# Kernel tuning notes

Measured on AMD Instinct MI355X. Metric: run time of the kernel, lower is better.

Reference implementation:

```python
import jax, jax.numpy as jnp
import numpy as np

DIM = 256
RATIO = 4
SCALE = 8
B, H, W = 16, 128, 128
EPS = 1e-5


def _conv(x, w, pad):
    return jax.lax.conv_general_dilated(
        x, w, window_strides=(1, 1), padding=[(pad, pad), (pad, pad)],
        dimension_numbers=('NCHW', 'OIHW', 'NCHW'))


def _haar_dwt(x):
    # pywt.dwt2(x, 'haar') on even-sized inputs == strided 2x2 sum/difference
    a = x[:, :, 0::2, 0::2]
    b = x[:, :, 0::2, 1::2]
    c = x[:, :, 1::2, 0::2]
    d = x[:, :, 1::2, 1::2]
    ll = (a + b + c + d) * 0.5
    lh = (a + b - c - d) * 0.5  # cH: high-pass along rows
    hl = (a - b + c - d) * 0.5  # cV: high-pass along cols
    hh = (a - b - c + d) * 0.5  # cD
    return jnp.concatenate([ll, lh, hl, hh], axis=1)


def setup_inputs() -> dict:
    key = jax.random.key(0)
    ks = jax.random.split(key, 16)
    dq = DIM // RATIO
    ds = DIM // SCALE
    s = 0.05
    return {
        'x': jax.random.normal(ks[0], (B, DIM, H, W), jnp.float32),
        'reduce_w': jax.random.normal(ks[1], (dq, DIM, 1, 1), jnp.float32) * s,
        'reduce_b': jnp.zeros((dq,), jnp.float32),
        'bn_g': jnp.ones((dq,), jnp.float32),
        'bn_b': jnp.zeros((dq,), jnp.float32),
        'bn_mean': jnp.zeros((dq,), jnp.float32),
        'bn_var': jnp.ones((dq,), jnp.float32),
        'conv_w': jax.random.normal(ks[2], (1, DIM, 1, 1), jnp.float32) * s,
        'conv1_w': jax.random.normal(ks[3], (DIM, DIM, 1, 1), jnp.float32) * s,
        'conv2_w': jax.random.normal(ks[4], (DIM, DIM, 3, 3), jnp.float32) * s,
        'conv3_w': jax.random.normal(ks[5], (DIM, DIM, 5, 5), jnp.float32) * s,
        'conv4_w': jax.random.normal(ks[6], (DIM, DIM, 7, 7), jnp.float32) * s,
        'channel_conv_w': jax.random.normal(ks[7], (DIM, DIM, 3, 3), jnp.float32) * s,
        'conv1x1_w': jax.random.normal(ks[8], (DIM, 6 * DIM, 3, 3), jnp.float32) * s,
        'ct1_w': jax.random.normal(ks[9], (ds, DIM, 1, 1), jnp.float32) * s,
        'ct1_b': jnp.zeros((ds,), jnp.float32),
        'ln_g': jnp.ones((ds,), jnp.float32),
        'ln_b': jnp.zeros((ds,), jnp.float32),
        'ct2_w': jax.random.normal(ks[10], (DIM, ds, 1, 1), jnp.float32) * s,
        'ct2_b': jnp.zeros((DIM,), jnp.float32),
        'proj_w': jax.random.normal(ks[11], (DIM, DIM, 1, 1), jnp.float32) * s,
    }


def reference(x, reduce_w, reduce_b, bn_g, bn_b, bn_mean, bn_var, conv_w,
              conv1_w, conv2_w, conv3_w, conv4_w, channel_conv_w, conv1x1_w,
              ct1_w, ct1_b, ln_g, ln_b, ct2_w, ct2_b, proj_w):
    # max-pool 2x2 stride 2
    p = jax.lax.reduce_window(x, -jnp.inf, jax.lax.max,
                              (1, 1, 2, 2), (1, 1, 2, 2), 'VALID')
    # reduce: 1x1 conv -> BN (inference) -> ReLU
    r = _conv(x, reduce_w, 0) + reduce_b[None, :, None, None]
    r = (r - bn_mean[None, :, None, None]) * jax.lax.rsqrt(bn_var + EPS)[None, :, None, None]
    r = jax.nn.relu(r * bn_g[None, :, None, None] + bn_b[None, :, None, None])
    # Haar DWT (original runs under no_grad: detached from autograd)
    qkv0 = jax.lax.stop_gradient(_haar_dwt(r))  # [B, DIM, H/2, W/2]
    qkv1 = _conv(qkv0, conv1_w, 0)
    qkv2 = _conv(qkv0, conv2_w, 1)
    qkv3 = _conv(qkv0, conv3_w, 2)
    qkv4 = _conv(qkv0, conv4_w, 3)
    qkv = _conv(jnp.concatenate([qkv0, qkv1, qkv2, qkv3, qkv4, p], axis=1),
                conv1x1_w, 1)  # [B, DIM, H/2, W/2]
    n = (H // 2) * (W // 2)
    # spatial attention weights: softmax over spatial positions
    content = _conv(qkv, conv_w, 0).reshape(B, n)          # [B, N]
    content = jax.nn.softmax(content, axis=1)
    channel = _conv(qkv, channel_conv_w, 1).reshape(B, DIM, n)  # [B, C, N]
    pooled = jnp.einsum('bcn,bn->bc', channel, content)[:, :, None, None]
    # channel transform: 1x1 -> LayerNorm over (C,1,1) -> ReLU -> 1x1
    t = _conv(pooled, ct1_w, 0) + ct1_b[None, :, None, None]
    mu = jnp.mean(t, axis=(1, 2, 3), keepdims=True)
    var = jnp.mean(jnp.square(t - mu), axis=(1, 2, 3), keepdims=True)
    t = (t - mu) * jax.lax.rsqrt(var + EPS)
    t = jax.nn.relu(t * ln_g[None, :, None, None] + ln_b[None, :, None, None])
    cw = _conv(t, ct2_w, 0) + ct2_b[None, :, None, None]  # [B, DIM, 1, 1]
    return _conv(qkv * cw, proj_w, 0)
```

## Files before the change

kernel.cpp:

```cpp
#include <hip/hip_runtime.h>
#include <stdint.h>


typedef __attribute__((ext_vector_type(8))) short bf16x8;
typedef __attribute__((ext_vector_type(4))) float f32x4;

#define EPS_ 1e-5f

#define GLOAD16(gp, lp)                                                        \
  __builtin_amdgcn_global_load_lds(                                            \
      (const __attribute__((address_space(1))) void*)(gp),                     \
      (__attribute__((address_space(3))) void*)(lp), 16, 0, 0)

__device__ __forceinline__ float bf2f(unsigned short u) {
  union { unsigned int u; float f; } c; c.u = ((unsigned int)u) << 16; return c.f;
}
__device__ __forceinline__ unsigned short f2bf(float f) {
  union { float f; unsigned int u; } c; c.f = f;
  return (unsigned short)((c.u + 0x7fffu + ((c.u >> 16) & 1u)) >> 16);
}
__device__ __forceinline__ void unpack8(uint4 v, float* f) {
  f[0]=bf2f((unsigned short)(v.x&0xffffu)); f[1]=bf2f((unsigned short)(v.x>>16));
  f[2]=bf2f((unsigned short)(v.y&0xffffu)); f[3]=bf2f((unsigned short)(v.y>>16));
  f[4]=bf2f((unsigned short)(v.z&0xffffu)); f[5]=bf2f((unsigned short)(v.z>>16));
  f[6]=bf2f((unsigned short)(v.w&0xffffu)); f[7]=bf2f((unsigned short)(v.w>>16));
}
__device__ __forceinline__ uint4 pack8(const float* f) {
  uint4 v;
  v.x = (unsigned)f2bf(f[0]) | ((unsigned)f2bf(f[1])<<16);
  v.y = (unsigned)f2bf(f[2]) | ((unsigned)f2bf(f[3])<<16);
  v.z = (unsigned)f2bf(f[4]) | ((unsigned)f2bf(f[5])<<16);
  v.w = (unsigned)f2bf(f[6]) | ((unsigned)f2bf(f[7])<<16);
  return v;
}

__global__ void k_repack(const float* __restrict__ src, unsigned short* __restrict__ dst,
                         int O, int Opad, int I, int T) {
  int gid = blockIdx.x * 256 + threadIdx.x;
  if (gid >= Opad * I * T) return;
  int i = gid % I; int r = gid / I; int o = r % Opad; int t = r / Opad;
  dst[gid] = (o < O) ? f2bf(src[((size_t)(o * I + i)) * T + t]) : (unsigned short)0;
}

__global__ void k_border_zero(unsigned short* __restrict__ buf, int PW, int PB, int C) {
  int IW = PW - 2 * PB;
  int nb = PW * PW - IW * IW;
  int per = C >> 3;
  int gid = blockIdx.x * 256 + threadIdx.x;
  if (gid >= 16 * nb * per) return;
  int cq = gid % per; int r = gid / per; int p = r % nb; int b = r / nb;
  int y, x;
  int top = PB * PW;
  if (p < top) { y = p / PW; x = p - y * PW; }
  else if (p < top + IW * 2 * PB) {
    int q = p - top; y = PB + q / (2 * PB); int rr = q % (2 * PB);
    x = (rr < PB) ? rr : (IW + rr);
  } else { int q = p - top - IW * 2 * PB; y = PB + IW + q / PW; x = q - (q / PW) * PW; }
  uint4 z; z.x = z.y = z.z = z.w = 0u;
  *(uint4*)&buf[(((size_t)b * PW + y) * PW + x) * C + cq * 8] = z;
}

__global__ void k_transpose_x(const float* __restrict__ x, unsigned short* __restrict__ xh) {
  int by = blockIdx.x; int b = by >> 7; int y = by & 127;
  int tid = threadIdx.x;
  __shared__ unsigned short lds[32 * 129];
  for (int c0 = 0; c0 < 256; c0 += 32) {
    #pragma unroll
    for (int i = 0; i < 16; ++i) {
      int e = i * 256 + tid; int ci = e >> 7, xx = e & 127;
      float v = x[(((size_t)b * 256 + c0 + ci) * 128 + y) * 128 + xx];
      lds[ci * 129 + xx] = f2bf(v);
    }
    __syncthreads();
    #pragma unroll
    for (int i2 = 0; i2 < 2; ++i2) {
      int e = i2 * 256 + tid; int pix = e >> 2, q = e & 3;
      unsigned int w0, w1, w2, w3;
      w0 = (unsigned)lds[(q*8+0)*129 + pix] | ((unsigned)lds[(q*8+1)*129 + pix] << 16);
      w1 = (unsigned)lds[(q*8+2)*129 + pix] | ((unsigned)lds[(q*8+3)*129 + pix] << 16);
      w2 = (unsigned)lds[(q*8+4)*129 + pix] | ((unsigned)lds[(q*8+5)*129 + pix] << 16);
      w3 = (unsigned)lds[(q*8+6)*129 + pix] | ((unsigned)lds[(q*8+7)*129 + pix] << 16);
      uint4 v; v.x = w0; v.y = w1; v.z = w2; v.w = w3;
      *(uint4*)&xh[(((size_t)b * 128 + y) * 128 + pix) * 256 + c0 + q * 8] = v;
    }
    __syncthreads();
  }
}

__global__ void k_maxpool(const unsigned short* __restrict__ xh, unsigned short* __restrict__ cat) {
  int gid = blockIdx.x * 256 + threadIdx.x;
  int cq = gid & 31; int pix = gid >> 5;
  int bb = pix >> 12; int yx = pix & 4095;
  int y = yx >> 6, xx2 = yx & 63;
  size_t base = (((size_t)bb * 128 + 2 * y) * 128 + 2 * xx2) * 256 + cq * 8;
  uint4 v00 = *(const uint4*)(xh + base);
  uint4 v01 = *(const uint4*)(xh + base + 256);
  uint4 v10 = *(const uint4*)(xh + base + 32768);
  uint4 v11 = *(const uint4*)(xh + base + 32768 + 256);
  float a[8], b8[8], c8[8], d8[8], m8[8];
  unpack8(v00, a); unpack8(v01, b8); unpack8(v10, c8); unpack8(v11, d8);
  #pragma unroll
  for (int j = 0; j < 8; ++j) m8[j] = fmaxf(fmaxf(a[j], b8[j]), fmaxf(c8[j], d8[j]));
  *(uint4*)(cat + (((size_t)bb * 4900 + (y + 3) * 70 + (xx2 + 3))) * 1536 + 1280 + cq * 8) = pack8(m8);
}

__global__ void k_haar(const unsigned short* __restrict__ rbn, unsigned short* __restrict__ cat) {
  int gid = blockIdx.x * 256 + threadIdx.x;
  int cq = gid & 7; int pix = gid >> 3;
  int bb = pix >> 12; int yx = pix & 4095;
  int y = yx >> 6, xx = yx & 63;
  size_t base = (((size_t)bb * 128 + 2 * y) * 128 + 2 * xx) * 64 + cq * 8;
  uint4 va = *(const uint4*)(rbn + base);
  uint4 vb = *(const uint4*)(rbn + base + 64);
  uint4 vc = *(const uint4*)(rbn + base + 8192);
  uint4 vd = *(const uint4*)(rbn + base + 8192 + 64);
  float a[8], b8[8], c8[8], d8[8], o[8];
  unpack8(va, a); unpack8(vb, b8); unpack8(vc, c8); unpack8(vd, d8);
  size_t ob = ((size_t)bb * 4900 + (y + 3) * 70 + (xx + 3)) * 1536 + cq * 8;
  #pragma unroll
  for (int j = 0; j < 8; ++j) o[j] = (a[j] + b8[j] + c8[j] + d8[j]) * 0.5f;
  *(uint4*)(cat + ob + 0)   = pack8(o);
  #pragma unroll
  for (int j = 0; j < 8; ++j) o[j] = (a[j] + b8[j] - c8[j] - d8[j]) * 0.5f;
  *(uint4*)(cat + ob + 64)  = pack8(o);
  #pragma unroll
  for (int j = 0; j < 8; ++j) o[j] = (a[j] - b8[j] + c8[j] - d8[j]) * 0.5f;
  *(uint4*)(cat + ob + 128) = pack8(o);
  #pragma unroll
  for (int j = 0; j < 8; ++j) o[j] = (a[j] - b8[j] - c8[j] + d8[j]) * 0.5f;
  *(uint4*)(cat + ob + 192) = pack8(o);
}

__global__ __launch_bounds__(512, 1) void k_conv_gemm256(
    const unsigned short* __restrict__ Wt, const unsigned short* __restrict__ Bf,
    int Cin, int Cstr, int cbase,
    int PW, int PB, int KH, int pad,
    unsigned long long wbstride,
    unsigned short* __restrict__ outb, int OCstr, int ocbase, int OPW, int OPB,
    float* __restrict__ outf, int mode) {
  const int tid = threadIdx.x, lane = tid & 63, w = tid >> 6;
  const int wm = w >> 2, wn = w & 3;
  const int nidx = (blockIdx.x & 7) * 32 + (blockIdx.x >> 3);
  const int bn = (nidx & 15) * 256;
  const int b = nidx >> 4;
  if (wbstride) Wt += (size_t)b * wbstride;
  extern __shared__ unsigned short S[];

  f32x4 zero4 = {0.f, 0.f, 0.f, 0.f};
  f32x4 acc[8][4];
  #pragma unroll
  for (int i = 0; i < 8; ++i)
    #pragma unroll
    for (int j = 0; j < 4; ++j) acc[i][j] = zero4;

  const int lq = lane >> 3, lc = lane & 7;
  const int lg = (lc - lq) & 7;
  const int pr = lg >> 2;
  const int ks = lg & 3;
  const unsigned short* aSt = Wt + (size_t)(w * 32 + 2 * lq + pr) * Cin + ks * 8;
  const size_t jA = (size_t)16 * Cin;
  const size_t bimg = (size_t)b * PW * PW;
  const unsigned short* bSt0; const unsigned short* bSt1;
  {
    int p = bn + w * 32 + 2 * lq + pr;
    bSt0 = Bf + (bimg + (size_t)((p >> 6) + PB) * PW + ((p & 63) + PB)) * Cstr + cbase + ks * 8;
    p += 16;
    bSt1 = Bf + (bimg + (size_t)((p >> 6) + PB) * PW + ((p & 63) + PB)) * Cstr + cbase + ks * 8;
  }
  const int dstA0 = w * 1024;
  const int dstB0 = 8192 + w * 1024;

  const int r = lane & 15, s4 = lane >> 4;
  const int ck = (((r & 1) * 4 + s4) + ((r >> 1) & 7)) & 7;
  const int lb = (r >> 1) * 64 + ck * 8;
  const int aOff = wm * 4096 + lb;
  const int bOff = 8192 + wn * 2048 + lb;

  const size_t MC = (size_t)256 * Cin;
  const int NT = (KH * KH * Cin) >> 5;

  const long long t0B = ((long long)(-pad) * PW + (-pad)) * (long long)Cstr;
  GLOAD16(aSt,             S + dstA0);
  GLOAD16(aSt + jA,        S + dstA0 + 512);
  GLOAD16(bSt0 + t0B,      S + dstB0);
  GLOAD16(bSt1 + t0B,      S + dstB0 + 512);
  GLOAD16(aSt + 32,        S + 16384 + dstA0);
  GLOAD16(aSt + jA + 32,   S + 16384 + dstA0 + 512);
  GLOAD16(bSt0 + t0B + 32, S + 16384 + dstB0);
  GLOAD16(bSt1 + t0B + 32, S + 16384 + dstB0 + 512);
  asm volatile("s_waitcnt vmcnt(4)" ::: "memory");
  __builtin_amdgcn_s_barrier();
  __builtin_amdgcn_sched_barrier(0);

  int kc2 = 64, ty2 = 0, tx2 = 0;
  for (int t = 0; t < NT; ++t) {
    const unsigned short* Sc = S + (t & 3) * 16384;
    unsigned short* Sn = (unsigned short*)S + ((t + 2) & 3) * 16384;
    const bool hn = (t + 2) < NT;
    long long offA = 0, offB = 0;
    if (hn) {
      offA = (long long)(ty2 * KH + tx2) * MC + kc2;
      offB = ((long long)(ty2 - pad) * PW + (tx2 - pad)) * (long long)Cstr + kc2;
      kc2 += 32;
      if (kc2 == Cin) { kc2 = 0; ++tx2; if (tx2 == KH) { tx2 = 0; ++ty2; } }
    }
    bf16x8 a[4], bb[4];
    #pragma unroll
    for (int mi = 0; mi < 4; ++mi) a[mi] = *(const bf16x8*)(Sc + aOff + mi * 512);
    #pragma unroll
    for (int ni = 0; ni < 4; ++ni) bb[ni] = *(const bf16x8*)(Sc + bOff + ni * 512);
    if (hn) {
      GLOAD16(aSt + offA,      Sn + dstA0);
      GLOAD16(aSt + jA + offA, Sn + dstA0 + 512);
    }
    __builtin_amdgcn_s_setprio(1);
    #pragma unroll
    for (int mi = 0; mi < 4; ++mi)
      #pragma unroll
      for (int ni = 0; ni < 4; ++ni)
        acc[mi][ni] = __builtin_amdgcn_mfma_f32_16x16x32_bf16(a[mi], bb[ni], acc[mi][ni], 0, 0, 0);
    __builtin_amdgcn_s_setprio(0);
    __builtin_amdgcn_s_barrier();
    #pragma unroll
    for (int mi = 0; mi < 4; ++mi) a[mi] = *(const bf16x8*)(Sc + aOff + (mi + 4) * 512);
    if (hn) {
      GLOAD16(bSt0 + offB, Sn + dstB0);
      GLOAD16(bSt1 + offB, Sn + dstB0 + 512);
    }
    __builtin_amdgcn_s_setprio(1);
    #pragma unroll
    for (int mi = 0; mi < 4; ++mi)
      #pragma unroll
      for (int ni = 0; ni < 4; ++ni)
        acc[mi + 4][ni] = __builtin_amdgcn_mfma_f32_16x16x32_bf16(a[mi], bb[ni], acc[mi + 4][ni], 0, 0, 0);
    __builtin_amdgcn_s_setprio(0);
    if (t + 1 < NT) {
      if (t + 2 < NT) { asm volatile("s_waitcnt vmcnt(4)" ::: "memory"); }
      else            { asm volatile("s_waitcnt vmcnt(0)" ::: "memory"); }
      __builtin_amdgcn_s_barrier();
      __builtin_amdgcn_sched_barrier(0);
    }
  }

  const size_t bimgO = (size_t)b * OPW * OPW;
  #pragma unroll
  for (int mi = 0; mi < 8; ++mi) {
    const int mf = wm * 128 + mi * 16 + (lane >> 4) * 4;
    #pragma unroll
    for (int ni = 0; ni < 4; ++ni) {
      const int n = bn + wn * 64 + ni * 16 + (lane & 15);
      if (mode == 2) {
        #pragma unroll
        for (int vv = 0; vv < 4; ++vv)
          outf[((size_t)b * 256 + mf + vv) * 4096 + n] = acc[mi][ni][vv];
      } else {
        const int oy = n >> 6, ox = n & 63;
        unsigned short h[4];
        #pragma unroll
        for (int vv = 0; vv < 4; ++vv) h[vv] = f2bf(acc[mi][ni][vv]);
        uint2 st; st.x = (unsigned)h[0] | ((unsigned)h[1] << 16);
        st.y = (unsigned)h[2] | ((unsigned)h[3] << 16);
        *(uint2*)&outb[(bimgO + (size_t)(oy + OPB) * OPW + (ox + OPB)) * OCstr + ocbase + mf] = st;
      }
    }
  }
}

__global__ __launch_bounds__(256) void k_conv_gemm(
    const unsigned short* __restrict__ Wt, const unsigned short* __restrict__ Bf,
    int M, int Mpad, int Cin, int Cstr, int cbase,
    int OW, int lgOW, int PW, int PB, int KH, int pad,
    unsigned long long wbstride,
    unsigned short* __restrict__ outb, int OCstr, int ocbase, int OPW, int OPB,
    float* __restrict__ outf, int mode,
    const float* __restrict__ rb, const float* __restrict__ bng, const float* __restrict__ bnb,
    const float* __restrict__ bnm, const float* __restrict__ bnv) {
  const int tid = threadIdx.x, lane = tid & 63, w = tid >> 6;
  const int wm = w >> 1, wn = w & 1;
  const int bm = blockIdx.y * 128, bn = blockIdx.x * 128;
  const int b = blockIdx.z;
  const int Npix = OW * OW;
  if (wbstride) Wt += (size_t)b * wbstride;

  __shared__ __align__(1024) unsigned short sA[128 * 32];
  __shared__ __align__(1024) unsigned short sB[128 * 32];

  f32x4 zero4 = {0.f, 0.f, 0.f, 0.f};
  f32x4 acc[4][4];
  #pragma unroll
  for (int i = 0; i < 4; ++i)
    #pragma unroll
    for (int j = 0; j < 4; ++j) acc[i][j] = zero4;

  const int srow = lane >> 2;
  const int slog = (lane & 3) ^ ((lane >> 3) & 3);
// ... 80 lines not shown
        *(uint2*)&outb[(bimgO + (size_t)(oy + OPB) * OPW + (ox + OPB)) * OCstr + ocbase + mf] = st;
      }
    }
  }
}

__global__ void k_content_logits(const unsigned short* __restrict__ qkv,
                                 const float* __restrict__ conv_w,
                                 float* __restrict__ logits) {
  int j = blockIdx.x, b = blockIdx.y, tid = threadIdx.x;
  __shared__ float wl[256];
  wl[tid] = conv_w[tid];
  __syncthreads();
  int pl = tid >> 3, kp = tid & 7;
  #pragma unroll
  for (int pass = 0; pass < 4; ++pass) {
    int p = j * 128 + pass * 32 + pl;
    int y = p >> 6, x = p & 63;
    const unsigned short* q = qkv + (((size_t)b * 66 + y + 1) * 66 + (x + 1)) * 256 + kp * 32;
    float s = 0.f;
    #pragma unroll
    for (int i = 0; i < 32; i += 8) {
      uint4 v = *(const uint4*)(q + i);
      float f[8]; unpack8(v, f);
      #pragma unroll
      for (int k = 0; k < 8; ++k) s += f[k] * wl[kp * 32 + i + k];
    }
    s += __shfl_down(s, 4, 8);
    s += __shfl_down(s, 2, 8);
    s += __shfl_down(s, 1, 8);
    if (kp == 0) logits[(size_t)b * 4096 + p] = s;
  }
}

__global__ void k_softmax4096(float* __restrict__ cont) {
  int b = blockIdx.x, tid = threadIdx.x;
  __shared__ float red[256];
  float sv[16]; float mx = -1e30f;
  #pragma unroll
  for (int j = 0; j < 16; ++j) { sv[j] = cont[(size_t)b * 4096 + j * 256 + tid]; mx = fmaxf(mx, sv[j]); }
  red[tid] = mx; __syncthreads();
  for (int s = 128; s > 0; s >>= 1) { if (tid < s) red[tid] = fmaxf(red[tid], red[tid + s]); __syncthreads(); }
  mx = red[0]; __syncthreads();
  float sum = 0.f;
  #pragma unroll
  for (int j = 0; j < 16; ++j) { sv[j] = expf(sv[j] - mx); sum += sv[j]; }
  red[tid] = sum; __syncthreads();
  for (int s = 128; s > 0; s >>= 1) { if (tid < s) red[tid] += red[tid + s]; __syncthreads(); }
  float inv = 1.f / red[0];
  #pragma unroll
  for (int j = 0; j < 16; ++j) cont[(size_t)b * 4096 + j * 256 + tid] = sv[j] * inv;
}

__global__ void k_pooled_part(const unsigned short* __restrict__ chn,
                              const float* __restrict__ content, float* __restrict__ ppart) {
  int j = blockIdx.x, b = blockIdx.y, c = threadIdx.x;
  const unsigned short* base = chn + (size_t)b * 4096 * 256 + c;
  const float* ct = content + (size_t)b * 4096;
  float acc = 0.f;
  int n0 = j * 128;
  for (int n = n0; n < n0 + 128; ++n)
    acc += bf2f(base[(size_t)n * 256]) * ct[n];
  ppart[((size_t)b * 32 + j) * 256 + c] = acc;
}
__global__ void k_pooled_red(const float* __restrict__ ppart, float* __restrict__ pooled) {
  int b = blockIdx.x, c = threadIdx.x;
  float s = 0.f;
  #pragma unroll
  for (int j = 0; j < 32; ++j) s += ppart[((size_t)b * 32 + j) * 256 + c];
  pooled[b * 256 + c] = s;
}

__global__ void k_ct(const float* __restrict__ pooled,
                     const float* __restrict__ ct1w, const float* __restrict__ ct1b,
                     const float* __restrict__ lng, const float* __restrict__ lnb,
                     const float* __restrict__ ct2w, const float* __restrict__ ct2b,
                     float* __restrict__ cw) {
  int b = blockIdx.x, tid = threadIdx.x;
  __shared__ float tt[32];
  __shared__ float stats[2];
  if (tid < 32) {
    float s = 0.f;
    const float* w = ct1w + tid * 256;
    const float* p = pooled + b * 256;
    for (int i = 0; i < 256; ++i) s += w[i] * p[i];
    tt[tid] = s + ct1b[tid];
  }
  __syncthreads();
  if (tid == 0) {
    float mu = 0.f;
    for (int j = 0; j < 32; ++j) mu += tt[j];
    mu *= (1.f / 32.f);
    float va = 0.f;
    for (int j = 0; j < 32; ++j) { float d = tt[j] - mu; va += d * d; }
    va *= (1.f / 32.f);
    stats[0] = mu; stats[1] = rsqrtf(va + EPS_);
  }
  __syncthreads();
  if (tid < 32) {
    float v = (tt[tid] - stats[0]) * stats[1];
    tt[tid] = fmaxf(v * lng[tid] + lnb[tid], 0.f);
  }
  __syncthreads();
  float s = 0.f;
  const float* w2 = ct2w + tid * 32;
  #pragma unroll
  for (int j = 0; j < 32; ++j) s += w2[j] * tt[j];
  cw[b * 256 + tid] = s + ct2b[tid];
}

__global__ void k_aproj(const float* __restrict__ projw, const float* __restrict__ cw,
                        unsigned short* __restrict__ aproj) {
  int gid = blockIdx.x * 256 + threadIdx.x;
  int b = gid >> 16; int oi = gid & 65535; int i = oi & 255;
  aproj[gid] = f2bf(projw[oi] * cw[b * 256 + i]);
}

extern "C" void kernel_launch(void* const* d_in, const int* in_sizes, int n_in,
                              void* d_out, int out_size, void* d_ws, size_t ws_size,
                              hipStream_t stream) {
  (void)in_sizes; (void)n_in; (void)out_size; (void)ws_size;
  const float* x        = (const float*)d_in[0];
  const float* reduce_w = (const float*)d_in[1];
  const float* reduce_b = (const float*)d_in[2];
  const float* bn_g     = (const float*)d_in[3];
  const float* bn_b     = (const float*)d_in[4];
  const float* bn_mean  = (const float*)d_in[5];
  const float* bn_var   = (const float*)d_in[6];
  const float* conv_w   = (const float*)d_in[7];
  const float* conv1_w  = (const float*)d_in[8];
  const float* conv2_w  = (const float*)d_in[9];
  const float* conv3_w  = (const float*)d_in[10];
  const float* conv4_w  = (const float*)d_in[11];
  const float* chconv_w = (const float*)d_in[12];
  const float* cat_w    = (const float*)d_in[13];
  const float* ct1_w    = (const float*)d_in[14];
  const float* ct1_b    = (const float*)d_in[15];
  const float* ln_g     = (const float*)d_in[16];
  const float* ln_b     = (const float*)d_in[17];
  const float* ct2_w    = (const float*)d_in[18];
  const float* ct2_b    = (const float*)d_in[19];
  const float* proj_w   = (const float*)d_in[20];

  static bool attr_done = false;
  if (!attr_done) {
    hipFuncSetAttribute(reinterpret_cast<const void*>(&k_conv_gemm256),
                        hipFuncAttributeMaxDynamicSharedMemorySize, 131072);
    attr_done = true;
  }

  char* wsp = (char*)d_ws;
  size_t off = 0;
  auto alloc = [&](size_t bytes) -> char* {
    char* p = wsp + off; off += (bytes + 255) & ~(size_t)255; return p;
  };
  unsigned short* XH    = (unsigned short*)alloc((size_t)16 * 16384 * 256 * 2);
  unsigned short* CAT   = (unsigned short*)alloc((size_t)16 * 4900 * 1536 * 2);
  unsigned short* RBN   = (unsigned short*)alloc((size_t)16 * 16384 * 64 * 2);
  unsigned short* CHN   = RBN;
  unsigned short* QKV   = (unsigned short*)alloc((size_t)16 * 4356 * 256 * 2);
  float*          CONT  = (float*)alloc((size_t)16 * 4096 * 4);
  float*          PPART = (float*)alloc((size_t)16 * 32 * 256 * 4);
  float*          POOL  = (float*)alloc(16 * 256 * 4);
  float*          CWB   = (float*)alloc(16 * 256 * 4);
  unsigned short* WR    = (unsigned short*)alloc((size_t)128 * 256 * 2);
  unsigned short* W1    = (unsigned short*)alloc((size_t)256 * 256 * 2);
  unsigned short* W2    = (unsigned short*)alloc((size_t)9 * 256 * 256 * 2);
  unsigned short* W3    = (unsigned short*)alloc((size_t)25 * 256 * 256 * 2);
  unsigned short* W4    = (unsigned short*)alloc((size_t)49 * 256 * 256 * 2);
  unsigned short* WC    = (unsigned short*)alloc((size_t)9 * 256 * 256 * 2);
  unsigned short* WCAT  = (unsigned short*)alloc((size_t)9 * 256 * 1536 * 2);
  unsigned short* APROJ = (unsigned short*)alloc((size_t)16 * 256 * 256 * 2);

  auto rp = [&](const float* s, unsigned short* d, int O, int Opad, int I, int T) {
    int tot = Opad * I * T;
    k_repack<<<(tot + 255) / 256, 256, 0, stream>>>(s, d, O, Opad, I, T);
  };
  rp(reduce_w, WR, 64, 128, 256, 1);
  rp(conv1_w, W1, 256, 256, 256, 1);
  rp(conv2_w, W2, 256, 256, 256, 9);
  rp(conv3_w, W3, 256, 256, 256, 25);
  rp(conv4_w, W4, 256, 256, 256, 49);
  rp(chconv_w, WC, 256, 256, 256, 9);
  rp(cat_w, WCAT, 256, 256, 1536, 9);

  k_border_zero<<<(16 * 804 * 192 + 255) / 256, 256, 0, stream>>>(CAT, 70, 3, 1536);
  k_border_zero<<<(16 * 260 * 32 + 255) / 256, 256, 0, stream>>>(QKV, 66, 1, 256);

  k_transpose_x<<<2048, 256, 0, stream>>>(x, XH);
  k_maxpool<<<8192, 256, 0, stream>>>(XH, CAT);

  dim3 blk(256);
  k_conv_gemm<<<dim3(128, 1, 16), blk, 0, stream>>>(WR, XH, 64, 128, 256, 256, 0,
      128, 7, 128, 0, 1, 0, 0ULL, RBN, 64, 0, 128, 0, nullptr, 1,
      reduce_b, bn_g, bn_b, bn_mean, bn_var);
  k_haar<<<2048, 256, 0, stream>>>(RBN, CAT);
  k_conv_gemm256<<<256, 512, 131072, stream>>>(W1, CAT, 256, 1536, 0,
      70, 3, 1, 0, 0ULL, CAT, 1536, 256, 70, 3, nullptr, 0);
  k_conv_gemm256<<<256, 512, 131072, stream>>>(W2, CAT, 256, 1536, 0,
      70, 3, 3, 1, 0ULL, CAT, 1536, 512, 70, 3, nullptr, 0);
  k_conv_gemm256<<<256, 512, 131072, stream>>>(W3, CAT, 256, 1536, 0,
      70, 3, 5, 2, 0ULL, CAT, 1536, 768, 70, 3, nullptr, 0);
  k_conv_gemm256<<<256, 512, 131072, stream>>>(W4, CAT, 256, 1536, 0,
      70, 3, 7, 3, 0ULL, CAT, 1536, 1024, 70, 3, nullptr, 0);
  k_conv_gemm256<<<256, 512, 131072, stream>>>(WCAT, CAT, 1536, 1536, 0,
      70, 3, 3, 1, 0ULL, QKV, 256, 0, 66, 1, nullptr, 0);
  k_content_logits<<<dim3(32, 16), blk, 0, stream>>>(QKV, conv_w, CONT);
  k_softmax4096<<<16, blk, 0, stream>>>(CONT);
  k_conv_gemm256<<<256, 512, 131072, stream>>>(WC, QKV, 256, 256, 0,
      66, 1, 3, 1, 0ULL, CHN, 256, 0, 64, 0, nullptr, 0);
  k_pooled_part<<<dim3(32, 16), blk, 0, stream>>>(CHN, CONT, PPART);
  k_pooled_red<<<16, blk, 0, stream>>>(PPART, POOL);
  k_ct<<<16, blk, 0, stream>>>(POOL, ct1_w, ct1_b, ln_g, ln_b, ct2_w, ct2_b, CWB);
  k_aproj<<<4096, 256, 0, stream>>>(proj_w, CWB, APROJ);
  k_conv_gemm256<<<256, 512, 131072, stream>>>(APROJ, QKV, 256, 256, 0,
      66, 1, 1, 0, 65536ULL, nullptr, 256, 0, 64, 0, (float*)d_out, 2);
}
```

Measured before the change: 1.459 ms.

## Shrink conv GEMM tiles to 256x128 with 256 threads and two blocks per CU

Changes the main implicit-GEMM conv kernel from 512-thread blocks computing 256x256 tiles with a 4-stage dynamic LDS ring to 256-thread blocks computing 256x128 tiles with a static double-buffered LDS of 48KB. The aim is two resident blocks per CU and twice as many blocks per launch, which should improve latency hiding and load balance. The prefetch now waits on vmcnt(0) every iteration and keeps only one stage in flight, so memory latency may be less well hidden. The B tile is reused across half as many output channels per load, raising global traffic relative to compute.

```diff
diff --git a/kernel.cpp b/kernel.cpp
--- a/kernel.cpp
+++ b/kernel.cpp
@@ -131,7 +131,7 @@
   *(uint4*)(cat + ob + 192) = pack8(o);
 }
 
-__global__ __launch_bounds__(512, 1) void k_conv_gemm256(
+__global__ __launch_bounds__(256, 2) void k_conv_gemm256(
     const unsigned short* __restrict__ Wt, const unsigned short* __restrict__ Bf,
     int Cin, int Cstr, int cbase,
     int PW, int PB, int KH, int pad,
@@ -139,12 +139,12 @@
     unsigned short* __restrict__ outb, int OCstr, int ocbase, int OPW, int OPB,
     float* __restrict__ outf, int mode) {
   const int tid = threadIdx.x, lane = tid & 63, w = tid >> 6;
-  const int wm = w >> 2, wn = w & 3;
-  const int nidx = (blockIdx.x & 7) * 32 + (blockIdx.x >> 3);
-  const int bn = (nidx & 15) * 256;
-  const int b = nidx >> 4;
+  const int wm = w >> 1, wn = w & 1;
+  const int swz = (blockIdx.x & 7) * 64 + (blockIdx.x >> 3);
+  const int bn = (swz & 31) * 128;
+  const int b = swz >> 5;
   if (wbstride) Wt += (size_t)b * wbstride;
-  extern __shared__ unsigned short S[];
+  __shared__ __align__(1024) unsigned short S[24576];
 
   f32x4 zero4 = {0.f, 0.f, 0.f, 0.f};
   f32x4 acc[8][4];
@@ -157,7 +157,7 @@
   const int lg = (lc - lq) & 7;
   const int pr = lg >> 2;
   const int ks = lg & 3;
-  const unsigned short* aSt = Wt + (size_t)(w * 32 + 2 * lq + pr) * Cin + ks * 8;
+  const unsigned short* aSt = Wt + (size_t)(w * 64 + 2 * lq + pr) * Cin + ks * 8;
   const size_t jA = (size_t)16 * Cin;
   const size_t bimg = (size_t)b * PW * PW;
   const unsigned short* bSt0; const unsigned short* bSt1;
@@ -167,8 +167,8 @@
     p += 16;
     bSt1 = Bf + (bimg + (size_t)((p >> 6) + PB) * PW + ((p & 63) + PB)) * Cstr + cbase + ks * 8;
   }
-  const int dstA0 = w * 1024;
-  const int dstB0 = 8192 + w * 1024;
+  const int dA = w * 2048;
+  const int dB = 8192 + w * 1024;
 
   const int r = lane & 15, s4 = lane >> 4;
   const int ck = (((r & 1) * 4 + s4) + ((r >> 1) & 7)) & 7;
@@ -180,63 +180,47 @@
   const int NT = (KH * KH * Cin) >> 5;
 
   const long long t0B = ((long long)(-pad) * PW + (-pad)) * (long long)Cstr;
-  GLOAD16(aSt,             S + dstA0);
-  GLOAD16(aSt + jA,        S + dstA0 + 512);
-  GLOAD16(bSt0 + t0B,      S + dstB0);
-  GLOAD16(bSt1 + t0B,      S + dstB0 + 512);
-  GLOAD16(aSt + 32,        S + 16384 + dstA0);
-  GLOAD16(aSt + jA + 32,   S + 16384 + dstA0 + 512);
-  GLOAD16(bSt0 + t0B + 32, S + 16384 + dstB0);
-  GLOAD16(bSt1 + t0B + 32, S + 16384 + dstB0 + 512);
-  asm volatile("s_waitcnt vmcnt(4)" ::: "memory");
+  GLOAD16(aSt,            S + dA);
+  GLOAD16(aSt + jA,       S + dA + 512);
+  GLOAD16(aSt + 2 * jA,   S + dA + 1024);
+  GLOAD16(aSt + 3 * jA,   S + dA + 1536);
+  GLOAD16(bSt0 + t0B,     S + dB);
+  GLOAD16(bSt1 + t0B,     S + dB + 512);
+  asm volatile("s_waitcnt vmcnt(0)" ::: "memory");
   __builtin_amdgcn_s_barrier();
   __builtin_amdgcn_sched_barrier(0);
 
-  int kc2 = 64, ty2 = 0, tx2 = 0;
+  int kcn = 0, tyn = 0, txn = 0;
   for (int t = 0; t < NT; ++t) {
-    const unsigned short* Sc = S + (t & 3) * 16384;
-    unsigned short* Sn = (unsigned short*)S + ((t + 2) & 3) * 16384;
-    const bool hn = (t + 2) < NT;
-    long long offA = 0, offB = 0;
+    const unsigned short* Sc = S + (t & 1) * 12288;
+    unsigned short* Sn = (unsigned short*)S + ((t + 1) & 1) * 12288;
+    const bool hn = (t + 1) < NT;
     if (hn) {
-      offA = (long long)(ty2 * KH + tx2) * MC + kc2;
-      offB = ((long long)(ty2 - pad) * PW + (tx2 - pad)) * (long long)Cstr + kc2;
-      kc2 += 32;
-      if (kc2 == Cin) { kc2 = 0; ++tx2; if (tx2 == KH) { tx2 = 0; ++ty2; } }
-    }
-    bf16x8 a[4], bb[4];
-    #pragma unroll
-    for (int mi = 0; mi < 4; ++mi) a[mi] = *(const bf16x8*)(Sc + aOff + mi * 512);
+      kcn += 32;
+      if (kcn == Cin) { kcn = 0; ++txn; if (txn == KH) { txn = 0; ++tyn; } }
+      const long long offA = (long long)(tyn * KH + txn) * MC + kcn;
+      const long long offB = ((long long)(tyn - pad) * PW + (txn - pad)) * (long long)Cstr + kcn;
+      GLOAD16(aSt + offA,          Sn + dA);
+      GLOAD16(aSt + offA + jA,     Sn + dA + 512);
+      GLOAD16(aSt + offA + 2 * jA, Sn + dA + 1024);
+      GLOAD16(aSt + offA + 3 * jA, Sn + dA + 1536);
+      GLOAD16(bSt0 + offB,         Sn + dB);
+      GLOAD16(bSt1 + offB,         Sn + dB + 512);
+    }
+    bf16x8 a[8], bb[4];
+    #pragma unroll
+    for (int mi = 0; mi < 8; ++mi) a[mi] = *(const bf16x8*)(Sc + aOff + mi * 512);
     #pragma unroll
     for (int ni = 0; ni < 4; ++ni) bb[ni] = *(const bf16x8*)(Sc + bOff + ni * 512);
-    if (hn) {
-      GLOAD16(aSt + offA,      Sn + dstA0);
-      GLOAD16(aSt + jA + offA, Sn + dstA0 + 512);
-    }
     __builtin_amdgcn_s_setprio(1);
     #pragma unroll
-    for (int mi = 0; mi < 4; ++mi)
+    for (int mi = 0; mi < 8; ++mi)
       #pragma unroll
       for (int ni = 0; ni < 4; ++ni)
         acc[mi][ni] = __builtin_amdgcn_mfma_f32_16x16x32_bf16(a[mi], bb[ni], acc[mi][ni], 0, 0, 0);
     __builtin_amdgcn_s_setprio(0);
-    __builtin_amdgcn_s_barrier();
-    #pragma unroll
-    for (int mi = 0; mi < 4; ++mi) a[mi] = *(const bf16x8*)(Sc + aOff + (mi + 4) * 512);
     if (hn) {
-      GLOAD16(bSt0 + offB, Sn + dstB0);
-      GLOAD16(bSt1 + offB, Sn + dstB0 + 512);
-    }
-    __builtin_amdgcn_s_setprio(1);
-    #pragma unroll
-    for (int mi = 0; mi < 4; ++mi)
-      #pragma unroll
-      for (int ni = 0; ni < 4; ++ni)
-        acc[mi + 4][ni] = __builtin_amdgcn_mfma_f32_16x16x32_bf16(a[mi], bb[ni], acc[mi + 4][ni], 0, 0, 0);
-    __builtin_amdgcn_s_setprio(0);
-    if (t + 1 < NT) {
-      if (t + 2 < NT) { asm volatile("s_waitcnt vmcnt(4)" ::: "memory"); }
-      else            { asm volatile("s_waitcnt vmcnt(0)" ::: "memory"); }
+      asm volatile("s_waitcnt vmcnt(0)" ::: "memory");
       __builtin_amdgcn_s_barrier();
       __builtin_amdgcn_sched_barrier(0);
     }
@@ -517,13 +501,6 @@
   const float* ct2_b    = (const float*)d_in[19];
   const float* proj_w   = (const float*)d_in[20];
 
-  static bool attr_done = false;
-  if (!attr_done) {
-    hipFuncSetAttribute(reinterpret_cast<const void*>(&k_conv_gemm256),
-                        hipFuncAttributeMaxDynamicSharedMemorySize, 131072);
-    attr_done = true;
-  }
-
   char* wsp = (char*)d_ws;
   size_t off = 0;
   auto alloc = [&](size_t bytes) -> char* {
@@ -570,24 +547,24 @@
       128, 7, 128, 0, 1, 0, 0ULL, RBN, 64, 0, 128, 0, nullptr, 1,
       reduce_b, bn_g, bn_b, bn_mean, bn_var);
   k_haar<<<2048, 256, 0, stream>>>(RBN, CAT);
-  k_conv_gemm256<<<256, 512, 131072, stream>>>(W1, CAT, 256, 1536, 0,
+  k_conv_gemm256<<<512, 256, 0, stream>>>(W1, CAT, 256, 1536, 0,
       70, 3, 1, 0, 0ULL, CAT, 1536, 256, 70, 3, nullptr, 0);
-  k_conv_gemm256<<<256, 512, 131072, stream>>>(W2, CAT, 256, 1536, 0,
+  k_conv_gemm256<<<512, 256, 0, stream>>>(W2, CAT, 256, 1536, 0,
       70, 3, 3, 1, 0ULL, CAT, 1536, 512, 70, 3, nullptr, 0);
-  k_conv_gemm256<<<256, 512, 131072, stream>>>(W3, CAT, 256, 1536, 0,
+  k_conv_gemm256<<<512, 256, 0, stream>>>(W3, CAT, 256, 1536, 0,
       70, 3, 5, 2, 0ULL, CAT, 1536, 768, 70, 3, nullptr, 0);
-  k_conv_gemm256<<<256, 512, 131072, stream>>>(W4, CAT, 256, 1536, 0,
+  k_conv_gemm256<<<512, 256, 0, stream>>>(W4, CAT, 256, 1536, 0,
       70, 3, 7, 3, 0ULL, CAT, 1536, 1024, 70, 3, nullptr, 0);
-  k_conv_gemm256<<<256, 512, 131072, stream>>>(WCAT, CAT, 1536, 1536, 0,
+  k_conv_gemm256<<<512, 256, 0, stream>>>(WCAT, CAT, 1536, 1536, 0,
       70, 3, 3, 1, 0ULL, QKV, 256, 0, 66, 1, nullptr, 0);
   k_content_logits<<<dim3(32, 16), blk, 0, stream>>>(QKV, conv_w, CONT);
   k_softmax4096<<<16, blk, 0, stream>>>(CONT);
-  k_conv_gemm256<<<256, 512, 131072, stream>>>(WC, QKV, 256, 256, 0,
+  k_conv_gemm256<<<512, 256, 0, stream>>>(WC, QKV, 256, 256, 0,
       66, 1, 3, 1, 0ULL, CHN, 256, 0, 64, 0, nullptr, 0);
   k_pooled_part<<<dim3(32, 16), blk, 0, stream>>>(CHN, CONT, PPART);
   k_pooled_red<<<16, blk, 0, stream>>>(PPART, POOL);
   k_ct<<<16, blk, 0, stream>>>(POOL, ct1_w, ct1_b, ln_g, ln_b, ct2_w, ct2_b, CWB);
   k_aproj<<<4096, 256, 0, stream>>>(proj_w, CWB, APROJ);
-  k_conv_gemm256<<<256, 512, 131072, stream>>>(APROJ, QKV, 256, 256, 0,
+  k_conv_gemm256<<<512, 256, 0, stream>>>(APROJ, QKV, 256, 256, 0,
       66, 1, 1, 0, 65536ULL, nullptr, 256, 0, 64, 0, (float*)d_out, 2);
 }
```

Measured after the change: 1.564 ms. 1.07x slower.

## Deepen GEMM pipeline to three LDS stages with register-double-buffered fragments

Applied to the files above, without the earlier changes.

Restructures the conv-GEMM main loop to prefetch three K-tiles ahead into the four-slot LDS ring. It also double-buffers the A/B MFMA fragments in registers, so the next tile's LDS reads overlap the current tile's MFMAs. The per-tile barrier count drops from two to one. Launch bounds are raised to request two blocks per CU. With 128 accumulator floats plus two full fragment sets, this risks heavy register spilling, and the 128KB LDS footprint likely prevents the second block from fitting anyway.

```diff
diff --git a/kernel.cpp b/kernel.cpp
--- a/kernel.cpp
+++ b/kernel.cpp
@@ -131,7 +131,7 @@
   *(uint4*)(cat + ob + 192) = pack8(o);
 }
 
-__global__ __launch_bounds__(512, 1) void k_conv_gemm256(
+__global__ __launch_bounds__(512, 2) void k_conv_gemm256(
     const unsigned short* __restrict__ Wt, const unsigned short* __restrict__ Bf,
     int Cin, int Cstr, int cbase,
     int PW, int PB, int KH, int pad,
@@ -144,7 +144,7 @@
   const int bn = (nidx & 15) * 256;
   const int b = nidx >> 4;
   if (wbstride) Wt += (size_t)b * wbstride;
-  extern __shared__ unsigned short S[];
+  extern __shared__ unsigned short Sb[];
 
   f32x4 zero4 = {0.f, 0.f, 0.f, 0.f};
   f32x4 acc[8][4];
@@ -167,8 +167,8 @@
     p += 16;
     bSt1 = Bf + (bimg + (size_t)((p >> 6) + PB) * PW + ((p & 63) + PB)) * Cstr + cbase + ks * 8;
   }
-  const int dstA0 = w * 1024;
-  const int dstB0 = 8192 + w * 1024;
+  const int dA = w * 1024;
+  const int dB = 8192 + w * 1024;
 
   const int r = lane & 15, s4 = lane >> 4;
   const int ck = (((r & 1) * 4 + s4) + ((r >> 1) & 7)) & 7;
@@ -180,67 +180,73 @@
   const int NT = (KH * KH * Cin) >> 5;
 
   const long long t0B = ((long long)(-pad) * PW + (-pad)) * (long long)Cstr;
-  GLOAD16(aSt,             S + dstA0);
-  GLOAD16(aSt + jA,        S + dstA0 + 512);
-  GLOAD16(bSt0 + t0B,      S + dstB0);
-  GLOAD16(bSt1 + t0B,      S + dstB0 + 512);
-  GLOAD16(aSt + 32,        S + 16384 + dstA0);
-  GLOAD16(aSt + jA + 32,   S + 16384 + dstA0 + 512);
-  GLOAD16(bSt0 + t0B + 32, S + 16384 + dstB0);
-  GLOAD16(bSt1 + t0B + 32, S + 16384 + dstB0 + 512);
+  #pragma unroll
+  for (int j = 0; j < 3; ++j) {
+    unsigned short* Sw = Sb + j * 16384;
+    GLOAD16(aSt + j * 32,        Sw + dA);
+    GLOAD16(aSt + j * 32 + jA,   Sw + dA + 512);
+    GLOAD16(bSt0 + t0B + j * 32, Sw + dB);
+    GLOAD16(bSt1 + t0B + j * 32, Sw + dB + 512);
+  }
   asm volatile("s_waitcnt vmcnt(4)" ::: "memory");
   __builtin_amdgcn_s_barrier();
   __builtin_amdgcn_sched_barrier(0);
 
-  int kc2 = 64, ty2 = 0, tx2 = 0;
-  for (int t = 0; t < NT; ++t) {
-    const unsigned short* Sc = S + (t & 3) * 16384;
-    unsigned short* Sn = (unsigned short*)S + ((t + 2) & 3) * 16384;
-    const bool hn = (t + 2) < NT;
-    long long offA = 0, offB = 0;
-    if (hn) {
-      offA = (long long)(ty2 * KH + tx2) * MC + kc2;
-      offB = ((long long)(ty2 - pad) * PW + (tx2 - pad)) * (long long)Cstr + kc2;
-      kc2 += 32;
-      if (kc2 == Cin) { kc2 = 0; ++tx2; if (tx2 == KH) { tx2 = 0; ++ty2; } }
-    }
-    bf16x8 a[4], bb[4];
-    #pragma unroll
-    for (int mi = 0; mi < 4; ++mi) a[mi] = *(const bf16x8*)(Sc + aOff + mi * 512);
-    #pragma unroll
-    for (int ni = 0; ni < 4; ++ni) bb[ni] = *(const bf16x8*)(Sc + bOff + ni * 512);
-    if (hn) {
-      GLOAD16(aSt + offA,      Sn + dstA0);
-      GLOAD16(aSt + jA + offA, Sn + dstA0 + 512);
-    }
-    __builtin_amdgcn_s_setprio(1);
-    #pragma unroll
-    for (int mi = 0; mi < 4; ++mi)
-      #pragma unroll
-      for (int ni = 0; ni < 4; ++ni)
-        acc[mi][ni] = __builtin_amdgcn_mfma_f32_16x16x32_bf16(a[mi], bb[ni], acc[mi][ni], 0, 0, 0);
-    __builtin_amdgcn_s_setprio(0);
-    __builtin_amdgcn_s_barrier();
-    #pragma unroll
-    for (int mi = 0; mi < 4; ++mi) a[mi] = *(const bf16x8*)(Sc + aOff + (mi + 4) * 512);
-    if (hn) {
-      GLOAD16(bSt0 + offB, Sn + dstB0);
-      GLOAD16(bSt1 + offB, Sn + dstB0 + 512);
-    }
-    __builtin_amdgcn_s_setprio(1);
-    #pragma unroll
-    for (int mi = 0; mi < 4; ++mi)
-      #pragma unroll
-      for (int ni = 0; ni < 4; ++ni)
-        acc[mi + 4][ni] = __builtin_amdgcn_mfma_f32_16x16x32_bf16(a[mi], bb[ni], acc[mi + 4][ni], 0, 0, 0);
-    __builtin_amdgcn_s_setprio(0);
-    if (t + 1 < NT) {
-      if (t + 2 < NT) { asm volatile("s_waitcnt vmcnt(4)" ::: "memory"); }
-      else            { asm volatile("s_waitcnt vmcnt(0)" ::: "memory"); }
-      __builtin_amdgcn_s_barrier();
-      __builtin_amdgcn_sched_barrier(0);
-    }
-  }
+  bf16x8 fa0[8], fb0[4], fa1[8], fb1[4];
+  #pragma unroll
+  for (int mi = 0; mi < 8; ++mi) fa0[mi] = *(const bf16x8*)(Sb + aOff + mi * 512);
+  #pragma unroll
+  for (int ni = 0; ni < 4; ++ni) fb0[ni] = *(const bf16x8*)(Sb + bOff + ni * 512);
+
+  int kcn = 96, tyn = 0, txn = 0;
+  int t = 0;
+
+#define TILE_BODY(CA, CB, NA, NB)                                              \
+  {                                                                            \
+    if (t + 3 < NT) {                                                          \
+      const long long offA = (long long)(tyn * KH + txn) * MC + kcn;           \
+      const long long offB = ((long long)(tyn - pad) * PW + (txn - pad)) *     \
+                                 (long long)Cstr + kcn;                        \
+      unsigned short* Sw = Sb + ((t + 3) & 3) * 16384;                         \
+      GLOAD16(aSt + offA,      Sw + dA);                                       \
+      GLOAD16(aSt + offA + jA, Sw + dA + 512);                                 \
+      GLOAD16(bSt0 + offB,     Sw + dB);                                       \
+      GLOAD16(bSt1 + offB,     Sw + dB + 512);                                 \
+      kcn += 32;                                                               \
+      if (kcn == Cin) { kcn = 0; ++txn; if (txn == KH) { txn = 0; ++tyn; } }   \
+    }                                                                          \
+    if (t + 1 < NT) {                                                          \
+      const unsigned short* Sp = Sb + ((t + 1) & 3) * 16384;                   \
+      _Pragma("unroll")                                                        \
+      for (int mi = 0; mi < 8; ++mi)                                           \
+        NA[mi] = *(const bf16x8*)(Sp + aOff + mi * 512);                       \
+      _Pragma("unroll")                                                        \
+      for (int ni = 0; ni < 4; ++ni)                                           \
+        NB[ni] = *(const bf16x8*)(Sp + bOff + ni * 512);                       \
+    }                                                                          \
+    __builtin_amdgcn_s_setprio(1);                                             \
+    _Pragma("unroll")                                                          \
+    for (int mi = 0; mi < 8; ++mi)                                             \
+      _Pragma("unroll")                                                        \
+      for (int ni = 0; ni < 4; ++ni)                                           \
+        acc[mi][ni] = __builtin_amdgcn_mfma_f32_16x16x32_bf16(                 \
+            CA[mi], CB[ni], acc[mi][ni], 0, 0, 0);                             \
+    __builtin_amdgcn_s_setprio(0);                                             \
+    if (t + 1 < NT) {                                                          \
+      if (t + 3 < NT) { asm volatile("s_waitcnt vmcnt(4)" ::: "memory"); }     \
+      else            { asm volatile("s_waitcnt vmcnt(0)" ::: "memory"); }     \
+      __builtin_amdgcn_s_barrier();                                            \
+      __builtin_amdgcn_sched_barrier(0);                                       \
+    }                                                                          \
+  }
+
+  while (true) {
+    TILE_BODY(fa0, fb0, fa1, fb1);
+    if (++t == NT) break;
+    TILE_BODY(fa1, fb1, fa0, fb0);
+    if (++t == NT) break;
+  }
+#undef TILE_BODY
 
   const size_t bimgO = (size_t)b * OPW * OPW;
   #pragma unroll
```

Result: slower. 1.499 ms (+2.7%).

## Fold 1x1 conv into concat conv weights and replace channel conv with correlation

Applied to the files above, without the earlier changes.

Folds conv1 (1x1) into the final 1536-channel 3x3 conv by precomputing combined weights, which removes one GEMM and shrinks the concat buffer to 1280 channels. It also replaces the full channel 3x3 conv plus pooling with a pooled formulation: it correlates qkv with shifted softmax weights per tap, then contracts with the channel conv weights. This removes a large 3x3 GEMM in exchange for small scalar kernels and a weight-folding kernel that runs every call. Folding before bf16 rounding slightly changes numerics.

```diff
diff --git a/kernel.cpp b/kernel.cpp
--- a/kernel.cpp
+++ b/kernel.cpp
@@ -40,6 +40,23 @@
   if (gid >= Opad * I * T) return;
   int i = gid % I; int r = gid / I; int o = r % Opad; int t = r / Opad;
   dst[gid] = (o < O) ? f2bf(src[((size_t)(o * I + i)) * T + t]) : (unsigned short)0;
+}
+
+__global__ void k_fold1(const float* __restrict__ catw, const float* __restrict__ w1,
+                        unsigned short* __restrict__ dst) {
+  int gid = blockIdx.x; int tid = threadIdx.x;
+  int iq = gid % 5; int o = (gid / 5) & 255; int t = gid / 1280;
+  int i = iq * 256 + tid;
+  float s;
+  if (i < 256) {
+    s = catw[((size_t)o * 1536 + i) * 9 + t];
+    const float* cw = catw + ((size_t)o * 1536 + 256) * 9 + t;
+    for (int m = 0; m < 256; ++m)
+      s += cw[(size_t)m * 9] * w1[m * 256 + i];
+  } else {
+    s = catw[((size_t)o * 1536 + i + 256) * 9 + t];
+  }
+  dst[((size_t)t * 256 + o) * 1280 + i] = f2bf(s);
 }
 
 __global__ void k_border_zero(unsigned short* __restrict__ buf, int PW, int PB, int C) {
@@ -101,7 +118,7 @@
   unpack8(v00, a); unpack8(v01, b8); unpack8(v10, c8); unpack8(v11, d8);
   #pragma unroll
   for (int j = 0; j < 8; ++j) m8[j] = fmaxf(fmaxf(a[j], b8[j]), fmaxf(c8[j], d8[j]));
-  *(uint4*)(cat + (((size_t)bb * 4900 + (y + 3) * 70 + (xx2 + 3))) * 1536 + 1280 + cq * 8) = pack8(m8);
+  *(uint4*)(cat + (((size_t)bb * 4900 + (y + 3) * 70 + (xx2 + 3))) * 1280 + 1024 + cq * 8) = pack8(m8);
 }
 
 __global__ void k_haar(const unsigned short* __restrict__ rbn, unsigned short* __restrict__ cat) {
@@ -116,7 +133,7 @@
   uint4 vd = *(const uint4*)(rbn + base + 8192 + 64);
   float a[8], b8[8], c8[8], d8[8], o[8];
   unpack8(va, a); unpack8(vb, b8); unpack8(vc, c8); unpack8(vd, d8);
-  size_t ob = ((size_t)bb * 4900 + (y + 3) * 70 + (xx + 3)) * 1536 + cq * 8;
+  size_t ob = ((size_t)bb * 4900 + (y + 3) * 70 + (xx + 3)) * 1280 + cq * 8;
   #pragma unroll
   for (int j = 0; j < 8; ++j) o[j] = (a[j] + b8[j] + c8[j] + d8[j]) * 0.5f;
   *(uint4*)(cat + ob + 0)   = pack8(o);
@@ -167,8 +184,8 @@
     p += 16;
     bSt1 = Bf + (bimg + (size_t)((p >> 6) + PB) * PW + ((p & 63) + PB)) * Cstr + cbase + ks * 8;
   }
-  const int dstA0 = w * 1024;
-  const int dstB0 = 8192 + w * 1024;
+  const int dA = w * 1024;
+  const int dB = 8192 + w * 1024;
 
   const int r = lane & 15, s4 = lane >> 4;
   const int ck = (((r & 1) * 4 + s4) + ((r >> 1) & 7)) & 7;
@@ -180,14 +197,14 @@
   const int NT = (KH * KH * Cin) >> 5;
 
   const long long t0B = ((long long)(-pad) * PW + (-pad)) * (long long)Cstr;
-  GLOAD16(aSt,             S + dstA0);
-  GLOAD16(aSt + jA,        S + dstA0 + 512);
-  GLOAD16(bSt0 + t0B,      S + dstB0);
-  GLOAD16(bSt1 + t0B,      S + dstB0 + 512);
-  GLOAD16(aSt + 32,        S + 16384 + dstA0);
-  GLOAD16(aSt + jA + 32,   S + 16384 + dstA0 + 512);
-  GLOAD16(bSt0 + t0B + 32, S + 16384 + dstB0);
-  GLOAD16(bSt1 + t0B + 32, S + 16384 + dstB0 + 512);
+  GLOAD16(aSt,             S + dA);
+  GLOAD16(aSt + jA,        S + dA + 512);
+  GLOAD16(bSt0 + t0B,      S + dB);
+  GLOAD16(bSt1 + t0B,      S + dB + 512);
+  GLOAD16(aSt + 32,        S + 16384 + dA);
+  GLOAD16(aSt + jA + 32,   S + 16384 + dA + 512);
+  GLOAD16(bSt0 + t0B + 32, S + 16384 + dB);
+  GLOAD16(bSt1 + t0B + 32, S + 16384 + dB + 512);
   asm volatile("s_waitcnt vmcnt(4)" ::: "memory");
   __builtin_amdgcn_s_barrier();
   __builtin_amdgcn_sched_barrier(0);
@@ -210,8 +227,8 @@
     #pragma unroll
     for (int ni = 0; ni < 4; ++ni) bb[ni] = *(const bf16x8*)(Sc + bOff + ni * 512);
     if (hn) {
-      GLOAD16(aSt + offA,      Sn + dstA0);
-      GLOAD16(aSt + jA + offA, Sn + dstA0 + 512);
+      GLOAD16(aSt + offA,      Sn + dA);
+      GLOAD16(aSt + jA + offA, Sn + dA + 512);
     }
     __builtin_amdgcn_s_setprio(1);
     #pragma unroll
@@ -224,8 +241,8 @@
     #pragma unroll
     for (int mi = 0; mi < 4; ++mi) a[mi] = *(const bf16x8*)(Sc + aOff + (mi + 4) * 512);
     if (hn) {
-      GLOAD16(bSt0 + offB, Sn + dstB0);
-      GLOAD16(bSt1 + offB, Sn + dstB0 + 512);
+      GLOAD16(bSt0 + offB, Sn + dB);
+      GLOAD16(bSt1 + offB, Sn + dB + 512);
     }
     __builtin_amdgcn_s_setprio(1);
     #pragma unroll
@@ -427,23 +444,54 @@
   for (int j = 0; j < 16; ++j) cont[(size_t)b * 4096 + j * 256 + tid] = sv[j] * inv;
 }
 
-__global__ void k_pooled_part(const unsigned short* __restrict__ chn,
-                              const float* __restrict__ content, float* __restrict__ ppart) {
-  int j = blockIdx.x, b = blockIdx.y, c = threadIdx.x;
-  const unsigned short* base = chn + (size_t)b * 4096 * 256 + c;
-  const float* ct = content + (size_t)b * 4096;
+__global__ void k_corr(const unsigned short* __restrict__ qkv,
+                       const float* __restrict__ cont, float* __restrict__ gpart) {
+  int j = blockIdx.x, b = blockIdx.y, i = threadIdx.x;
+  __shared__ float cl[640];
+  for (int e = i; e < 640; e += 256) {
+    int gy = j * 8 - 1 + (e >> 6);
+    cl[e] = (gy >= 0 && gy < 64) ? cont[(size_t)b * 4096 + gy * 64 + (e & 63)] : 0.f;
+  }
+  __syncthreads();
+  float g[9] = {0.f, 0.f, 0.f, 0.f, 0.f, 0.f, 0.f, 0.f, 0.f};
+  for (int ry = 0; ry < 8; ++ry) {
+    int y = j * 8 + ry;
+    for (int x = 0; x < 64; ++x) {
+      float qv = bf2f(qkv[(((size_t)b * 66 + y + 1) * 66 + (x + 1)) * 256 + i]);
+      #pragma unroll
+      for (int ky = 0; ky < 3; ++ky) {
+        int ly = ry - ky + 2;
+        #pragma unroll
+        for (int kx = 0; kx < 3; ++kx) {
+          int nx = x - kx + 1;
+          if ((unsigned)nx < 64u) g[ky * 3 + kx] += qv * cl[ly * 64 + nx];
+        }
+      }
+    }
+  }
+  size_t base = ((size_t)b * 8 + j) * 2304 + i;
+  #pragma unroll
+  for (int t = 0; t < 9; ++t) gpart[base + t * 256] = g[t];
+}
+
+__global__ void k_pooled_g(const float* __restrict__ gpart,
+                           const float* __restrict__ wc, float* __restrict__ pooled) {
+  int b = blockIdx.x, c = threadIdx.x;
+  __shared__ float Gs[2304];
+  for (int e = c; e < 2304; e += 256) {
+    float s = 0.f;
+    #pragma unroll
+    for (int j = 0; j < 8; ++j) s += gpart[((size_t)b * 8 + j) * 2304 + e];
+    Gs[e] = s;
+  }
+  __syncthreads();
   float acc = 0.f;
-  int n0 = j * 128;
-  for (int n = n0; n < n0 + 128; ++n)
-    acc += bf2f(base[(size_t)n * 256]) * ct[n];
-  ppart[((size_t)b * 32 + j) * 256 + c] = acc;
-}
-__global__ void k_pooled_red(const float* __restrict__ ppart, float* __restrict__ pooled) {
-  int b = blockIdx.x, c = threadIdx.x;
-  float s = 0.f;
-  #pragma unroll
-  for (int j = 0; j < 32; ++j) s += ppart[((size_t)b * 32 + j) * 256 + c];
-  pooled[b * 256 + c] = s;
+  const float* w = wc + (size_t)c * 2304;
+  for (int i = 0; i < 256; ++i)
+    #pragma unroll
+    for (int t = 0; t < 9; ++t)
+      acc += w[i * 9 + t] * Gs[t * 256 + i];
+  pooled[b * 256 + c] = acc;
 }
 
 __global__ void k_ct(const float* __restrict__ pooled,
@@ -530,21 +578,18 @@
     char* p = wsp + off; off += (bytes + 255) & ~(size_t)255; return p;
   };
   unsigned short* XH    = (unsigned short*)alloc((size_t)16 * 16384 * 256 * 2);
-  unsigned short* CAT   = (unsigned short*)alloc((size_t)16 * 4900 * 1536 * 2);
+  unsigned short* CAT   = (unsigned short*)alloc((size_t)16 * 4900 * 1280 * 2);
   unsigned short* RBN   = (unsigned short*)alloc((size_t)16 * 16384 * 64 * 2);
-  unsigned short* CHN   = RBN;
   unsigned short* QKV   = (unsigned short*)alloc((size_t)16 * 4356 * 256 * 2);
   float*          CONT  = (float*)alloc((size_t)16 * 4096 * 4);
-  float*          PPART = (float*)alloc((size_t)16 * 32 * 256 * 4);
+  float*          GPART = (float*)alloc((size_t)16 * 8 * 2304 * 4);
   float*          POOL  = (float*)alloc(16 * 256 * 4);
   float*          CWB   = (float*)alloc(16 * 256 * 4);
   unsigned short* WR    = (unsigned short*)alloc((size_t)128 * 256 * 2);
-  unsigned short* W1    = (unsigned short*)alloc((size_t)256 * 256 * 2);
   unsigned short* W2    = (unsigned short*)alloc((size_t)9 * 256 * 256 * 2);
   unsigned short* W3    = (unsigned short*)alloc((size_t)25 * 256 * 256 * 2);
   unsigned short* W4    = (unsigned short*)alloc((size_t)49 * 256 * 256 * 2);
-  unsigned short* WC    = (unsigned short*)alloc((size_t)9 * 256 * 256 * 2);
-  unsigned short* WCAT  = (unsigned short*)alloc((size_t)9 * 256 * 1536 * 2);
+  unsigned short* WBIG  = (unsigned short*)alloc((size_t)9 * 256 * 1280 * 2);
   unsigned short* APROJ = (unsigned short*)alloc((size_t)16 * 256 * 256 * 2);
 
   auto rp = [&](const float* s, unsigned short* d, int O, int Opad, int I, int T) {
@@ -552,14 +597,12 @@
     k_repack<<<(tot + 255) / 256, 256, 0, stream>>>(s, d, O, Opad, I, T);
   };
   rp(reduce_w, WR, 64, 128, 256, 1);
-  rp(conv1_w, W1, 256, 256, 256, 1);
   rp(conv2_w, W2, 256, 256, 256, 9);
   rp(conv3_w, W3, 256, 256, 256, 25);
   rp(conv4_w, W4, 256, 256, 256, 49);
-  rp(chconv_w, WC, 256, 256, 256, 9);
-  rp(cat_w, WCAT, 256, 256, 1536, 9);
-
-  k_border_zero<<<(16 * 804 * 192 + 255) / 256, 256, 0, stream>>>(CAT, 70, 3, 1536);
+  k_fold1<<<9 * 256 * 5, 256, 0, stream>>>(cat_w, conv1_w, WBIG);
+
+  k_border_zero<<<(16 * 804 * 160 + 255) / 256, 256, 0, stream>>>(CAT, 70, 3, 1280);
   k_border_zero<<<(16 * 260 * 32 + 255) / 256, 256, 0, stream>>>(QKV, 66, 1, 256);
 
   k_transpose_x<<<2048, 256, 0, stream>>>(x, XH);
@@ -570,22 +613,18 @@
       128, 7, 128, 0, 1, 0, 0ULL, RBN, 64, 0, 128, 0, nullptr, 1,
       reduce_b, bn_g, bn_b, bn_mean, bn_var);
   k_haar<<<2048, 256, 0, stream>>>(RBN, CAT);
-  k_conv_gemm256<<<256, 512, 131072, stream>>>(W1, CAT, 256, 1536, 0,
-      70, 3, 1, 0, 0ULL, CAT, 1536, 256, 70, 3, nullptr, 0);
-  k_conv_gemm256<<<256, 512, 131072, stream>>>(W2, CAT, 256, 1536, 0,
-      70, 3, 3, 1, 0ULL, CAT, 1536, 512, 70, 3, nullptr, 0);
-  k_conv_gemm256<<<256, 512, 131072, stream>>>(W3, CAT, 256, 1536, 0,
-      70, 3, 5, 2, 0ULL, CAT, 1536, 768, 70, 3, nullptr, 0);
-  k_conv_gemm256<<<256, 512, 131072, stream>>>(W4, CAT, 256, 1536, 0,
-      70, 3, 7, 3, 0ULL, CAT, 1536, 1024, 70, 3, nullptr, 0);
-  k_conv_gemm256<<<256, 512, 131072, stream>>>(WCAT, CAT, 1536, 1536, 0,
+  k_conv_gemm256<<<256, 512, 131072, stream>>>(W2, CAT, 256, 1280, 0,
+      70, 3, 3, 1, 0ULL, CAT, 1280, 256, 70, 3, nullptr, 0);
+  k_conv_gemm256<<<256, 512, 131072, stream>>>(W3, CAT, 256, 1280, 0,
+      70, 3, 5, 2, 0ULL, CAT, 1280, 512, 70, 3, nullptr, 0);
+  k_conv_gemm256<<<256, 512, 131072, stream>>>(W4, CAT, 256, 1280, 0,
+      70, 3, 7, 3, 0ULL, CAT, 1280, 768, 70, 3, nullptr, 0);
+  k_conv_gemm256<<<256, 512, 131072, stream>>>(WBIG, CAT, 1280, 1280, 0,
       70, 3, 3, 1, 0ULL, QKV, 256, 0, 66, 1, nullptr, 0);
   k_content_logits<<<dim3(32, 16), blk, 0, stream>>>(QKV, conv_w, CONT);
   k_softmax4096<<<16, blk, 0, stream>>>(CONT);
-  k_conv_gemm256<<<256, 512, 131072, stream>>>(WC, QKV, 256, 256, 0,
-      66, 1, 3, 1, 0ULL, CHN, 256, 0, 64, 0, nullptr, 0);
-  k_pooled_part<<<dim3(32, 16), blk, 0, stream>>>(CHN, CONT, PPART);
-  k_pooled_red<<<16, blk, 0, stream>>>(PPART, POOL);
+  k_corr<<<dim3(8, 16), blk, 0, stream>>>(QKV, CONT, GPART);
+  k_pooled_g<<<16, blk, 0, stream>>>(GPART, chconv_w, POOL);
   k_ct<<<16, blk, 0, stream>>>(POOL, ct1_w, ct1_b, ln_g, ln_b, ct2_w, ct2_b, CWB);
   k_aproj<<<4096, 256, 0, stream>>>(proj_w, CWB, APROJ);
   k_conv_gemm256<<<256, 512, 131072, stream>>>(APROJ, QKV, 256, 256, 0,
```

Measured after the change: 1.599 ms. 1.1x slower.
